# Kernel optimization log

Measured on AMD Instinct MI355X. Metric: run time of the kernel, lower is better.

Reference implementation:

```python
import jax, jax.numpy as jnp
import numpy as np

N_NODES = 400000
N_EDGES = 800000
DIM = 128
N_LAYER = 5
ATOM_VOCAB = 119   # len(possible_atomic_num_list)
CHIR_VOCAB = 4     # len(possible_chirality_list)
BN_EPS = 1e-5


def setup_inputs() -> dict:
    key = jax.random.key(0)
    ks = jax.random.split(key, 12)
    x = jax.random.randint(ks[0], (N_NODES, 2), 0, 4, dtype=jnp.int64 if jax.config.read('jax_enable_x64') else jnp.int32).astype(jnp.int32)
    edge_index = jax.random.randint(ks[1], (2, N_EDGES), 0, N_NODES).astype(jnp.int32)
    edge_attr = jax.random.randint(ks[2], (N_EDGES, 1), 0, 4).astype(jnp.int32)
    s = 0.02
    emb_atom = jax.random.normal(ks[3], (ATOM_VOCAB, DIM), jnp.float32) * s
    emb_chir = jax.random.normal(ks[4], (CHIR_VOCAB, DIM), jnp.float32) * s
    W1 = jax.random.normal(ks[5], (N_LAYER, DIM, DIM), jnp.float32) * s
    b1 = jnp.zeros((N_LAYER, DIM), jnp.float32)
    W2 = jax.random.normal(ks[6], (N_LAYER, DIM, DIM), jnp.float32) * s
    b2 = jnp.zeros((N_LAYER, DIM), jnp.float32)
    gamma = jnp.ones((N_LAYER, DIM), jnp.float32)
    beta = jnp.zeros((N_LAYER, DIM), jnp.float32)
    return {"x": x, "edge_index": edge_index, "edge_attr": edge_attr,
            "emb_atom": emb_atom, "emb_chir": emb_chir,
            "W1": W1, "b1": b1, "W2": W2, "b2": b2,
            "gamma": gamma, "beta": beta}


def _batch_norm_train(z, g, b):
    # BatchNorm1d in training mode: batch statistics over node axis
    mean = jnp.mean(z, axis=0)
    var = jnp.mean(jnp.square(z - mean), axis=0)  # biased var, as torch BN
    return (z - mean) * jax.lax.rsqrt(var + BN_EPS) * g + b


def reference(x, edge_index, edge_attr, emb_atom, emb_chir, W1, b1, W2, b2, gamma, beta):
    # summed per-column node embeddings (drop_ratio=0 -> dropout is identity)
    h = emb_atom[x[:, 0]] + emb_chir[x[:, 1]]           # [N, D]
    src, dst = edge_index[0], edge_index[1]
    n = h.shape[0]
    L = W1.shape[0]
    for l in range(L):
        # GINConv, eps=0: mlp((1+eps)*h_i + sum_{j->i} h_j)
        agg = jax.ops.segment_sum(h[src], dst, num_segments=n)  # gather-scatter
        z = h + agg
        z = jax.nn.relu(z @ W1[l] + b1[l]) @ W2[l] + b2[l]       # MLP([D, D, D])
        z = _batch_norm_train(z, gamma[l], beta[l])
        if l < L - 1:
            z = jax.nn.relu(z)
        h = z
    return h
```

## Files before the change

### kernel.cpp

```cpp
#include <hip/hip_runtime.h>
#include <hip/hip_bf16.h>

#define N_NODES 400000
#define N_EDGES 800000
#define DIM 128
#define NLAYER 5
#define BN_EPS 1e-5f

typedef _Float16 half8 __attribute__((ext_vector_type(8)));
typedef _Float16 half4 __attribute__((ext_vector_type(4)));
typedef float f32x4 __attribute__((ext_vector_type(4)));

__global__ __launch_bounds__(256) void k_embed(const int* __restrict__ x,
                                               const float* __restrict__ ea,
                                               const float* __restrict__ ec,
                                               _Float16* __restrict__ out) {
  int idx = blockIdx.x * 256 + threadIdx.x;
  int i = idx >> 4, c8 = (idx & 15) * 8;
  int av = x[2 * i], cv = x[2 * i + 1];
  float4 a0 = *(const float4*)(ea + (size_t)av * DIM + c8);
  float4 a1 = *(const float4*)(ea + (size_t)av * DIM + c8 + 4);
  float4 c0 = *(const float4*)(ec + (size_t)cv * DIM + c8);
  float4 c1 = *(const float4*)(ec + (size_t)cv * DIM + c8 + 4);
  half8 r;
  r[0] = (_Float16)(a0.x + c0.x); r[1] = (_Float16)(a0.y + c0.y);
  r[2] = (_Float16)(a0.z + c0.z); r[3] = (_Float16)(a0.w + c0.w);
  r[4] = (_Float16)(a1.x + c1.x); r[5] = (_Float16)(a1.y + c1.y);
  r[6] = (_Float16)(a1.z + c1.z); r[7] = (_Float16)(a1.w + c1.w);
  *(half8*)(out + (size_t)i * DIM + c8) = r;
}

__global__ __launch_bounds__(256) void k_hist(const int* __restrict__ dst, int* __restrict__ cnt) {
  int e = blockIdx.x * 256 + threadIdx.x;
  if (e < N_EDGES) atomicAdd(&cnt[dst[e]], 1);
}

__global__ __launch_bounds__(256) void k_scan1(const int* __restrict__ cnt, int* __restrict__ rp,
                                               int* __restrict__ part) {
  __shared__ int sm[256];
  int t = threadIdx.x;
  int base = blockIdx.x * 1024 + t * 4;
  int v0 = 0, v1 = 0, v2 = 0, v3 = 0;
  if (base + 4 <= N_NODES) {
    int4 v = *(const int4*)(cnt + base);
    v0 = v.x; v1 = v.y; v2 = v.z; v3 = v.w;
  } else {
    if (base     < N_NODES) v0 = cnt[base];
    if (base + 1 < N_NODES) v1 = cnt[base + 1];
    if (base + 2 < N_NODES) v2 = cnt[base + 2];
    if (base + 3 < N_NODES) v3 = cnt[base + 3];
  }
  int s = v0 + v1 + v2 + v3;
  sm[t] = s;
  __syncthreads();
  for (int off = 1; off < 256; off <<= 1) {
    int add = (t >= off) ? sm[t - off] : 0;
    __syncthreads();
    sm[t] += add;
    __syncthreads();
  }
  int incl = sm[t];
  int ex = incl - s;
  if (t == 255) part[blockIdx.x] = incl;
  if (base     < N_NODES) rp[base]     = ex;
  if (base + 1 < N_NODES) rp[base + 1] = ex + v0;
  if (base + 2 < N_NODES) rp[base + 2] = ex + v0 + v1;
  if (base + 3 < N_NODES) rp[base + 3] = ex + v0 + v1 + v2;
}

__global__ __launch_bounds__(512) void k_scan2(int* __restrict__ part, int nb) {
  __shared__ int sm[512];
  int t = threadIdx.x;
  int v = (t < nb) ? part[t] : 0;
  sm[t] = v;
  __syncthreads();
  for (int off = 1; off < 512; off <<= 1) {
    int add = (t >= off) ? sm[t - off] : 0;
    __syncthreads();
    sm[t] += add;
    __syncthreads();
  }
  if (t < nb) part[t] = sm[t] - v;
}

__global__ __launch_bounds__(256) void k_scan3(int* __restrict__ rp, const int* __restrict__ part) {
  int i = blockIdx.x * 256 + threadIdx.x;
  if (i < N_NODES) rp[i] += part[i >> 10];
  if (i == 0) rp[N_NODES] = N_EDGES;
}

__global__ __launch_bounds__(256) void k_scatter(const int* __restrict__ src, const int* __restrict__ dst,
                                                 const int* __restrict__ rp, int* __restrict__ fill,
                                                 int* __restrict__ es) {
  int e = blockIdx.x * 256 + threadIdx.x;
  if (e < N_EDGES) {
    int d = dst[e];
    int slot = rp[d] + atomicAdd(&fill[d], 1);
    es[slot] = src[e];
  }
}

__global__ __launch_bounds__(128) void k_wprep(const float* __restrict__ W1, const float* __restrict__ W2,
                                               _Float16* __restrict__ wt) {
  int b = blockIdx.x;
  int l = b >> 8, mat = (b >> 7) & 1, c = b & 127;
  int k = threadIdx.x;
  const float* W = mat ? W2 : W1;
  float v = W[(size_t)l * DIM * DIM + (size_t)k * DIM + c];
  wt[((size_t)(l * 2 + mat) * DIM + c) * DIM + k] = (_Float16)v;
}

template <int UA>
__global__ __launch_bounds__(256) void k_aggx(const _Float16* __restrict__ P, const int* __restrict__ rp,
                                              const int* __restrict__ es, const float* __restrict__ affine,
                                              _Float16* __restrict__ X) {
  const int lane = threadIdx.x & 63;
  const int g = lane >> 4, gl = lane & 15;
  const int wid = (blockIdx.x * 256 + threadIdx.x) >> 6;
  const int nid = wid * 4 + g;
  const int c8 = gl * 8;

  float a[8], c[8];
  if (UA) {
    float4 t0 = *(const float4*)(affine + c8);
    float4 t1 = *(const float4*)(affine + c8 + 4);
    float4 u0 = *(const float4*)(affine + DIM + c8);
    float4 u1 = *(const float4*)(affine + DIM + c8 + 4);
    a[0] = t0.x; a[1] = t0.y; a[2] = t0.z; a[3] = t0.w;
    a[4] = t1.x; a[5] = t1.y; a[6] = t1.z; a[7] = t1.w;
    c[0] = u0.x; c[1] = u0.y; c[2] = u0.z; c[3] = u0.w;
    c[4] = u1.x; c[5] = u1.y; c[6] = u1.z; c[7] = u1.w;
  }
  const int e0 = rp[nid], e1 = rp[nid + 1];

  half8 sv = *(const half8*)(P + (size_t)nid * DIM + c8);
  float sx[8];
#pragma unroll
  for (int i = 0; i < 8; ++i) {
    float v = (float)sv[i];
    sx[i] = UA ? fmaxf(fmaf(a[i], v, c[i]), 0.f) : v;
  }
  for (int base = e0; base < e1; base += 16) {
    int n = e1 - base; if (n > 16) n = 16;
    int esr = (base + gl < e1) ? es[base + gl] : 0;
    for (int j = 0; j < n; j += 4) {
      int s0 = __shfl(esr, (g << 4) + j);
      int s1 = __shfl(esr, (g << 4) + j + 1);
      int s2 = __shfl(esr, (g << 4) + j + 2);
      int s3 = __shfl(esr, (g << 4) + j + 3);
      float w1 = (j + 1 < n) ? 1.f : 0.f;
      float w2 = (j + 2 < n) ? 1.f : 0.f;
      float w3 = (j + 3 < n) ? 1.f : 0.f;
      half8 v0 = *(const half8*)(P + (size_t)s0 * DIM + c8);
      half8 v1 = *(const half8*)(P + (size_t)s1 * DIM + c8);
      half8 v2 = *(const half8*)(P + (size_t)s2 * DIM + c8);
      half8 v3 = *(const half8*)(P + (size_t)s3 * DIM + c8);
#pragma unroll
      for (int i = 0; i < 8; ++i) {
        float f0 = (float)v0[i], f1 = (float)v1[i];
        float f2 = (float)v2[i], f3 = (float)v3[i];
        if (UA) {
          f0 = fmaxf(fmaf(a[i], f0, c[i]), 0.f);
          f1 = fmaxf(fmaf(a[i], f1, c[i]), 0.f);
          f2 = fmaxf(fmaf(a[i], f2, c[i]), 0.f);
          f3 = fmaxf(fmaf(a[i], f3, c[i]), 0.f);
        }
        sx[i] += f0 + w1 * f1 + w2 * f2 + w3 * f3;
      }
    }
  }
  half8 r;
#pragma unroll
  for (int i = 0; i < 8; ++i) r[i] = (_Float16)sx[i];
  *(half8*)(X + (size_t)nid * DIM + c8) = r;
}

__global__ __launch_bounds__(256) void k_mlp(const _Float16* __restrict__ X,
                                             const _Float16* __restrict__ wt,
                                             const float* __restrict__ b1, const float* __restrict__ b2,
                                             _Float16* __restrict__ Z, float* __restrict__ stats) {
  __shared__ _Float16 sh[16384 + 64 * DIM];
  _Float16* wbuf = sh;
  _Float16* tb   = sh + 16384;

  const int tid = threadIdx.x;
  const int lane = tid & 63, w = tid >> 6;
  const int l15 = lane & 15, h = lane >> 4;
  const half8* wg = (const half8*)wt;

#pragma unroll
  for (int i = 0; i < 8; ++i) {
    int h8 = i * 256 + tid;
    half8 v = wg[h8];
    int cc = h8 >> 4, k8 = h8 & 15;
    int hidx = (cc * DIM + k8 * 8) ^ ((cc & 7) << 3);
    *(half8*)(wbuf + hidx) = v;
  }

  const int row = blockIdx.x * 64 + 16 * w + l15;
  const size_t rbase = (size_t)row * DIM;
  half8 xf[4];
#pragma unroll
  for (int kt = 0; kt < 4; ++kt)
    xf[kt] = *(const half8*)(X + rbase + kt * 32 + 8 * h);
  __syncthreads();

#pragma unroll
  for (int ct = 0; ct < 8; ++ct) {
    int n = ct * 16 + l15;
    float bv = b1[n];
    f32x4 acc = {bv, bv, bv, bv};
#pragma unroll
    for (int kt = 0; kt < 4; ++kt) {
      int hidx = (n * DIM + kt * 32 + 8 * h) ^ ((n & 7) << 3);
      half8 bf = *(const half8*)(wbuf + hidx);
      acc = __builtin_amdgcn_mfma_f32_16x16x32_f16(xf[kt], bf, acc, 0, 0, 0);
    }
#pragma unroll
    for (int r = 0; r < 4; ++r) {
      int lr = 16 * w + 4 * h + r;
      int ti = (lr * DIM + n) ^ ((lr & 7) << 3);
      tb[ti] = (_Float16)fmaxf(acc[r], 0.f);
    }
  }
  __syncthreads();

#pragma unroll
  for (int i = 0; i < 8; ++i) {
    int h8 = 2048 + i * 256 + tid;
    half8 v = wg[h8];
    int idx8 = h8 & 2047;
    int cc = idx8 >> 4, k8 = idx8 & 15;
    int hidx = (cc * DIM + k8 * 8) ^ ((cc & 7) << 3);
    *(half8*)(wbuf + hidx) = v;
  }
  half8 tf[4];
#pragma unroll
  for (int kt = 0; kt < 4; ++kt) {
    int lr = 16 * w + l15;
    int ti = (lr * DIM + kt * 32 + 8 * h) ^ ((lr & 7) << 3);
    tf[kt] = *(const half8*)(tb + ti);
  }
  __syncthreads();

  float sa[8], qa[8];
#pragma unroll
  for (int ct = 0; ct < 8; ++ct) {
    int n = ct * 16 + l15;
    float bv = b2[n];
    f32x4 acc = {bv, bv, bv, bv};
#pragma unroll
    for (int kt = 0; kt < 4; ++kt) {
      int hidx = (n * DIM + kt * 32 + 8 * h) ^ ((n & 7) << 3);
      half8 bf = *(const half8*)(wbuf + hidx);
      acc = __builtin_amdgcn_mfma_f32_16x16x32_f16(tf[kt], bf, acc, 0, 0, 0);
    }
    float s = 0.f, q = 0.f;
#pragma unroll
    for (int r = 0; r < 4; ++r) {
      int lr = 16 * w + 4 * h + r;
      float y = acc[r];
      int ti = (lr * DIM + n) ^ ((lr & 7) << 3);
      tb[ti] = (_Float16)y;
      s += y; q += y * y;
    }
    sa[ct] = s; qa[ct] = q;
  }
  __syncthreads();

  float* sst = (float*)sh;
  sst[tid] = 0.f;
  __syncthreads();
#pragma unroll
  for (int ct = 0; ct < 8; ++ct) {
    float s = sa[ct], q = qa[ct];
    s += __shfl_xor(s, 16); s += __shfl_xor(s, 32);
    q += __shfl_xor(q, 16); q += __shfl_xor(q, 32);
    if (h == 0) {
      int n = ct * 16 + l15;
      atomicAdd(&sst[n], s);
      atomicAdd(&sst[DIM + n], q);
    }
  }
  __syncthreads();

#pragma unroll
  for (int i = 0; i < 4; ++i) {
    int chunk = i * 256 + tid;
    int lr = chunk >> 4, k8 = chunk & 15;
    int ti = (lr * DIM + k8 * 8) ^ ((lr & 7) << 3);
    half8 v = *(const half8*)(tb + ti);
    *(half8*)(Z + (size_t)(blockIdx.x * 64 + lr) * DIM + k8 * 8) = v;
  }
  atomicAdd(&stats[(blockIdx.x & 63) * 256 + tid], sst[tid]);
}

__global__ __launch_bounds__(128) void k_fin(const float* __restrict__ stats, const float* __restrict__ gamma,
                                             const float* __restrict__ beta, float* __restrict__ affine) {
  int c = threadIdx.x;
  float s = 0.f, q = 0.f;
  for (int i = 0; i < 64; ++i) {
    s += stats[i * 256 + c];
    q += stats[i * 256 + DIM + c];
  }
  float mean = s / (float)N_NODES;
  float var = q / (float)N_NODES - mean * mean;
  float inv = 1.f / sqrtf(var + BN_EPS);
  float a = gamma[c] * inv;
  affine[c] = a;
  affine[DIM + c] = beta[c] - mean * a;
}

__global__ __launch_bounds__(256) void k_out(const _Float16* __restrict__ z, const float* __restrict__ affine,
                                             float* __restrict__ out) {
  int idx = blockIdx.x * 256 + threadIdx.x;
  int c4 = (idx & 31) * 4;
  half4 v = *(const half4*)(z + (size_t)idx * 4);
  float4 a = *(const float4*)(affine + c4);
  float4 c = *(const float4*)(affine + DIM + c4);
  float4 r;
  r.x = fmaf(a.x, (float)v[0], c.x); r.y = fmaf(a.y, (float)v[1], c.y);
  r.z = fmaf(a.z, (float)v[2], c.z); r.w = fmaf(a.w, (float)v[3], c.w);
  *(float4*)(out + (size_t)idx * 4) = r;
}

extern "C" void kernel_launch(void* const* d_in, const int* in_sizes, int n_in,
                              void* d_out, int out_size, void* d_ws, size_t ws_size,
                              hipStream_t stream) {
  const int*   x     = (const int*)d_in[0];
  const int*   ei    = (const int*)d_in[1];
  const float* ea    = (const float*)d_in[3];
  const float* ec    = (const float*)d_in[4];
  const float* W1    = (const float*)d_in[5];
  const float* b1    = (const float*)d_in[6];
  const float* W2    = (const float*)d_in[7];
  const float* b2    = (const float*)d_in[8];
  const float* gamma = (const float*)d_in[9];
  const float* beta  = (const float*)d_in[10];
  const int* src = ei;
  const int* dst = ei + N_EDGES;

  char* ws = (char*)d_ws;
  size_t off = 0;
  auto take = [&](size_t b) { char* p = ws + off; off += (b + 255) & ~(size_t)255; return p; };
  _Float16* Z0     = (_Float16*)take((size_t)N_NODES * DIM * 2);
  _Float16* Z1     = (_Float16*)take((size_t)N_NODES * DIM * 2);
  _Float16* X      = (_Float16*)take((size_t)N_NODES * DIM * 2);
  _Float16* wt     = (_Float16*)take((size_t)NLAYER * 2 * DIM * DIM * 2);
  int*      rp     = (int*)take((size_t)(N_NODES + 1) * 4);
  int*      fill   = (int*)take((size_t)N_NODES * 4);
  int*      es     = (int*)take((size_t)N_EDGES * 4);
  int*      part   = (int*)take(4096);
  float*    stats  = (float*)take(64 * 256 * 4);
  float*    affine = (float*)take(256 * 4);
  if (off > ws_size) return;

  const int NB1 = (N_NODES + 1023) / 1024;

  hipMemsetAsync(fill, 0, (size_t)N_NODES * 4, stream);
  k_hist<<<(N_EDGES + 255) / 256, 256, 0, stream>>>(dst, fill);
  k_scan1<<<NB1, 256, 0, stream>>>(fill, rp, part);
  k_scan2<<<1, 512, 0, stream>>>(part, NB1);
  k_scan3<<<(N_NODES + 255) / 256, 256, 0, stream>>>(rp, part);
  hipMemsetAsync(fill, 0, (size_t)N_NODES * 4, stream);
  k_scatter<<<(N_EDGES + 255) / 256, 256, 0, stream>>>(src, dst, rp, fill, es);

  k_embed<<<N_NODES * 16 / 256, 256, 0, stream>>>(x, ea, ec, Z0);
  k_wprep<<<NLAYER * 2 * DIM, DIM, 0, stream>>>(W1, W2, wt);

  _Float16* pin = Z0;
  _Float16* pout = Z1;
  for (int l = 0; l < NLAYER; ++l) {
    if (l == 0)
      k_aggx<0><<<N_NODES / 16, 256, 0, stream>>>(pin, rp, es, affine, X);
    else
      k_aggx<1><<<N_NODES / 16, 256, 0, stream>>>(pin, rp, es, affine, X);
    hipMemsetAsync(stats, 0, 64 * 256 * 4, stream);
    k_mlp<<<N_NODES / 64, 256, 0, stream>>>(X, wt + (size_t)l * 2 * DIM * DIM,
                                            b1 + l * DIM, b2 + l * DIM, pout, stats);
    k_fin<<<1, DIM, 0, stream>>>(stats, gamma + l * DIM, beta + l * DIM, affine);
    _Float16* t = pin; pin = pout; pout = t;
  }
  k_out<<<N_NODES * 32 / 256, 256, 0, stream>>>(pin, affine, (float*)d_out);
}
```

Measured before the change: 1.189 ms.

## Fuse neighbor aggregation into the MLP kernel, eliminating the X intermediate buffer

Merges the gather-sum aggregation kernel into the per-layer MLP kernel. Each thread now accumulates its node's neighbor features directly in the MFMA A-fragment layout (4 chunks of 8 halves), so the X intermediate is no longer written to or read back from HBM. The cost is a different gather pattern: each 16-lane group handles a single row, and lanes loop serially over edges with per-lane variable trip counts. This may cause wave divergence and lower memory-level parallelism than the old 4-wide shuffled gather, and it raises register pressure.

New measurement: 1.193 ms. Within noise of the previous version (+0.4%).

```diff
diff --git a/kernel.cpp b/kernel.cpp
--- a/kernel.cpp
+++ b/kernel.cpp
@@ -111,74 +111,13 @@
 }
 
 template <int UA>
-__global__ __launch_bounds__(256) void k_aggx(const _Float16* __restrict__ P, const int* __restrict__ rp,
-                                              const int* __restrict__ es, const float* __restrict__ affine,
-                                              _Float16* __restrict__ X) {
-  const int lane = threadIdx.x & 63;
-  const int g = lane >> 4, gl = lane & 15;
-  const int wid = (blockIdx.x * 256 + threadIdx.x) >> 6;
-  const int nid = wid * 4 + g;
-  const int c8 = gl * 8;
-
-  float a[8], c[8];
-  if (UA) {
-    float4 t0 = *(const float4*)(affine + c8);
-    float4 t1 = *(const float4*)(affine + c8 + 4);
-    float4 u0 = *(const float4*)(affine + DIM + c8);
-    float4 u1 = *(const float4*)(affine + DIM + c8 + 4);
-    a[0] = t0.x; a[1] = t0.y; a[2] = t0.z; a[3] = t0.w;
-    a[4] = t1.x; a[5] = t1.y; a[6] = t1.z; a[7] = t1.w;
-    c[0] = u0.x; c[1] = u0.y; c[2] = u0.z; c[3] = u0.w;
-    c[4] = u1.x; c[5] = u1.y; c[6] = u1.z; c[7] = u1.w;
-  }
-  const int e0 = rp[nid], e1 = rp[nid + 1];
-
-  half8 sv = *(const half8*)(P + (size_t)nid * DIM + c8);
-  float sx[8];
-#pragma unroll
-  for (int i = 0; i < 8; ++i) {
-    float v = (float)sv[i];
-    sx[i] = UA ? fmaxf(fmaf(a[i], v, c[i]), 0.f) : v;
-  }
-  for (int base = e0; base < e1; base += 16) {
-    int n = e1 - base; if (n > 16) n = 16;
-    int esr = (base + gl < e1) ? es[base + gl] : 0;
-    for (int j = 0; j < n; j += 4) {
-      int s0 = __shfl(esr, (g << 4) + j);
-      int s1 = __shfl(esr, (g << 4) + j + 1);
-      int s2 = __shfl(esr, (g << 4) + j + 2);
-      int s3 = __shfl(esr, (g << 4) + j + 3);
-      float w1 = (j + 1 < n) ? 1.f : 0.f;
-      float w2 = (j + 2 < n) ? 1.f : 0.f;
-      float w3 = (j + 3 < n) ? 1.f : 0.f;
-      half8 v0 = *(const half8*)(P + (size_t)s0 * DIM + c8);
-      half8 v1 = *(const half8*)(P + (size_t)s1 * DIM + c8);
-      half8 v2 = *(const half8*)(P + (size_t)s2 * DIM + c8);
-      half8 v3 = *(const half8*)(P + (size_t)s3 * DIM + c8);
-#pragma unroll
-      for (int i = 0; i < 8; ++i) {
-        float f0 = (float)v0[i], f1 = (float)v1[i];
-        float f2 = (float)v2[i], f3 = (float)v3[i];
-        if (UA) {
-          f0 = fmaxf(fmaf(a[i], f0, c[i]), 0.f);
-          f1 = fmaxf(fmaf(a[i], f1, c[i]), 0.f);
-          f2 = fmaxf(fmaf(a[i], f2, c[i]), 0.f);
-          f3 = fmaxf(fmaf(a[i], f3, c[i]), 0.f);
-        }
-        sx[i] += f0 + w1 * f1 + w2 * f2 + w3 * f3;
-      }
-    }
-  }
-  half8 r;
-#pragma unroll
-  for (int i = 0; i < 8; ++i) r[i] = (_Float16)sx[i];
-  *(half8*)(X + (size_t)nid * DIM + c8) = r;
-}
-
-__global__ __launch_bounds__(256) void k_mlp(const _Float16* __restrict__ X,
-                                             const _Float16* __restrict__ wt,
-                                             const float* __restrict__ b1, const float* __restrict__ b2,
-                                             _Float16* __restrict__ Z, float* __restrict__ stats) {
+__global__ __launch_bounds__(256) void k_layer(const _Float16* __restrict__ P,
+                                               const int* __restrict__ rp,
+                                               const int* __restrict__ es,
+                                               const float* __restrict__ affine,
+                                               const _Float16* __restrict__ wt,
+                                               const float* __restrict__ b1, const float* __restrict__ b2,
+                                               _Float16* __restrict__ Z, float* __restrict__ stats) {
   __shared__ _Float16 sh[16384 + 64 * DIM];
   _Float16* wbuf = sh;
   _Float16* tb   = sh + 16384;
@@ -197,30 +136,77 @@
     *(half8*)(wbuf + hidx) = v;
   }
 
+  float af[4][8], cf[4][8];
+  if (UA) {
+#pragma unroll
+    for (int kt = 0; kt < 4; ++kt) {
+      int k0 = kt * 32 + 8 * h;
+      float4 t0 = *(const float4*)(affine + k0);
+      float4 t1 = *(const float4*)(affine + k0 + 4);
+      float4 u0 = *(const float4*)(affine + DIM + k0);
+      float4 u1 = *(const float4*)(affine + DIM + k0 + 4);
+      af[kt][0] = t0.x; af[kt][1] = t0.y; af[kt][2] = t0.z; af[kt][3] = t0.w;
+      af[kt][4] = t1.x; af[kt][5] = t1.y; af[kt][6] = t1.z; af[kt][7] = t1.w;
+      cf[kt][0] = u0.x; cf[kt][1] = u0.y; cf[kt][2] = u0.z; cf[kt][3] = u0.w;
+      cf[kt][4] = u1.x; cf[kt][5] = u1.y; cf[kt][6] = u1.z; cf[kt][7] = u1.w;
+    }
+  }
+
   const int row = blockIdx.x * 64 + 16 * w + l15;
-  const size_t rbase = (size_t)row * DIM;
+  const size_t rbase = (size_t)row * DIM + 8 * h;
+  const int e0 = rp[row], e1 = rp[row + 1];
+  float acc[4][8];
+#pragma unroll
+  for (int kt = 0; kt < 4; ++kt) {
+    half8 sv = *(const half8*)(P + rbase + kt * 32);
+#pragma unroll
+    for (int i = 0; i < 8; ++i) {
+      float v = (float)sv[i];
+      acc[kt][i] = UA ? fmaxf(fmaf(af[kt][i], v, cf[kt][i]), 0.f) : v;
+    }
+  }
+  for (int e = e0; e < e1; ++e) {
+    const size_t nb = (size_t)es[e] * DIM + 8 * h;
+    half8 v0 = *(const half8*)(P + nb);
+    half8 v1 = *(const half8*)(P + nb + 32);
+    half8 v2 = *(const half8*)(P + nb + 64);
+    half8 v3 = *(const half8*)(P + nb + 96);
+#pragma unroll
+    for (int i = 0; i < 8; ++i) {
+      float f0 = (float)v0[i], f1 = (float)v1[i];
+      float f2 = (float)v2[i], f3 = (float)v3[i];
+      if (UA) {
+        f0 = fmaxf(fmaf(af[0][i], f0, cf[0][i]), 0.f);
+        f1 = fmaxf(fmaf(af[1][i], f1, cf[1][i]), 0.f);
+        f2 = fmaxf(fmaf(af[2][i], f2, cf[2][i]), 0.f);
+        f3 = fmaxf(fmaf(af[3][i], f3, cf[3][i]), 0.f);
+      }
+      acc[0][i] += f0; acc[1][i] += f1; acc[2][i] += f2; acc[3][i] += f3;
+    }
+  }
   half8 xf[4];
 #pragma unroll
   for (int kt = 0; kt < 4; ++kt)
-    xf[kt] = *(const half8*)(X + rbase + kt * 32 + 8 * h);
+#pragma unroll
+    for (int i = 0; i < 8; ++i) xf[kt][i] = (_Float16)acc[kt][i];
   __syncthreads();
 
 #pragma unroll
   for (int ct = 0; ct < 8; ++ct) {
     int n = ct * 16 + l15;
     float bv = b1[n];
-    f32x4 acc = {bv, bv, bv, bv};
+    f32x4 acc1 = {bv, bv, bv, bv};
 #pragma unroll
     for (int kt = 0; kt < 4; ++kt) {
       int hidx = (n * DIM + kt * 32 + 8 * h) ^ ((n & 7) << 3);
       half8 bf = *(const half8*)(wbuf + hidx);
-      acc = __builtin_amdgcn_mfma_f32_16x16x32_f16(xf[kt], bf, acc, 0, 0, 0);
+      acc1 = __builtin_amdgcn_mfma_f32_16x16x32_f16(xf[kt], bf, acc1, 0, 0, 0);
     }
 #pragma unroll
     for (int r = 0; r < 4; ++r) {
       int lr = 16 * w + 4 * h + r;
       int ti = (lr * DIM + n) ^ ((lr & 7) << 3);
-      tb[ti] = (_Float16)fmaxf(acc[r], 0.f);
+      tb[ti] = (_Float16)fmaxf(acc1[r], 0.f);
     }
   }
   __syncthreads();
@@ -248,18 +234,18 @@
   for (int ct = 0; ct < 8; ++ct) {
     int n = ct * 16 + l15;
     float bv = b2[n];
-    f32x4 acc = {bv, bv, bv, bv};
+    f32x4 acc2 = {bv, bv, bv, bv};
 #pragma unroll
     for (int kt = 0; kt < 4; ++kt) {
       int hidx = (n * DIM + kt * 32 + 8 * h) ^ ((n & 7) << 3);
       half8 bf = *(const half8*)(wbuf + hidx);
-      acc = __builtin_amdgcn_mfma_f32_16x16x32_f16(tf[kt], bf, acc, 0, 0, 0);
+      acc2 = __builtin_amdgcn_mfma_f32_16x16x32_f16(tf[kt], bf, acc2, 0, 0, 0);
     }
     float s = 0.f, q = 0.f;
 #pragma unroll
     for (int r = 0; r < 4; ++r) {
       int lr = 16 * w + 4 * h + r;
-      float y = acc[r];
+      float y = acc2[r];
       int ti = (lr * DIM + n) ^ ((lr & 7) << 3);
       tb[ti] = (_Float16)y;
       s += y; q += y * y;
@@ -345,7 +331,6 @@
   auto take = [&](size_t b) { char* p = ws + off; off += (b + 255) & ~(size_t)255; return p; };
   _Float16* Z0     = (_Float16*)take((size_t)N_NODES * DIM * 2);
   _Float16* Z1     = (_Float16*)take((size_t)N_NODES * DIM * 2);
-  _Float16* X      = (_Float16*)take((size_t)N_NODES * DIM * 2);
   _Float16* wt     = (_Float16*)take((size_t)NLAYER * 2 * DIM * DIM * 2);
   int*      rp     = (int*)take((size_t)(N_NODES + 1) * 4);
   int*      fill   = (int*)take((size_t)N_NODES * 4);
@@ -371,13 +356,15 @@
   _Float16* pin = Z0;
   _Float16* pout = Z1;
   for (int l = 0; l < NLAYER; ++l) {
+    hipMemsetAsync(stats, 0, 64 * 256 * 4, stream);
     if (l == 0)
-      k_aggx<0><<<N_NODES / 16, 256, 0, stream>>>(pin, rp, es, affine, X);
+      k_layer<0><<<N_NODES / 64, 256, 0, stream>>>(pin, rp, es, affine,
+                                                   wt + (size_t)l * 2 * DIM * DIM,
+                                                   b1 + l * DIM, b2 + l * DIM, pout, stats);
     else
-      k_aggx<1><<<N_NODES / 16, 256, 0, stream>>>(pin, rp, es, affine, X);
-    hipMemsetAsync(stats, 0, 64 * 256 * 4, stream);
-    k_mlp<<<N_NODES / 64, 256, 0, stream>>>(X, wt + (size_t)l * 2 * DIM * DIM,
-                                            b1 + l * DIM, b2 + l * DIM, pout, stats);
+      k_layer<1><<<N_NODES / 64, 256, 0, stream>>>(pin, rp, es, affine,
+                                                   wt + (size_t)l * 2 * DIM * DIM,
+                                                   b1 + l * DIM, b2 + l * DIM, pout, stats);
     k_fin<<<1, DIM, 0, stream>>>(stats, gamma + l * DIM, beta + l * DIM, affine);
     _Float16* t = pin; pin = pout; pout = t;
   }
```
